# Kernel tuning notes

Measured on AMD Instinct MI355X. Metric: run time of the kernel, lower is better.

## Reference

```python
import jax, jax.numpy as jnp
import numpy as np

SHIFT = 1
EPS = 1e-5

def setup_inputs() -> dict:
    key = jax.random.key(0)
    k1, k2, k3, k4, k5, k6 = jax.random.split(key, 6)
    B, C, H, Wd = 64, 512, 28, 28
    Cout = 512
    return {
        "x": jax.random.normal(k1, (B, C, H, Wd), dtype=jnp.float32),
        "W": jax.random.normal(k2, (Cout, C), dtype=jnp.float32) * 0.05,
        "gamma": jax.random.uniform(k3, (Cout,), dtype=jnp.float32) + 0.5,
        "beta": jax.random.normal(k4, (Cout,), dtype=jnp.float32) * 0.1,
        "running_mean": jax.random.normal(k5, (Cout,), dtype=jnp.float32) * 0.1,
        "running_var": jax.random.uniform(k6, (Cout,), dtype=jnp.float32) + 0.5,
    }

def reference(x, W, gamma, beta, running_mean, running_var):
    # Group-wise spatial shift: split channels into 4 groups, roll each.
    Cg = x.shape[1] // 4
    x1 = jnp.roll(x[:, 0*Cg:1*Cg], -SHIFT, axis=2)  # up
    x2 = jnp.roll(x[:, 1*Cg:2*Cg],  SHIFT, axis=2)  # down
    x3 = jnp.roll(x[:, 2*Cg:3*Cg], -SHIFT, axis=3)  # left
    x4 = jnp.roll(x[:, 3*Cg:4*Cg],  SHIFT, axis=3)  # right
    shifted = jnp.concatenate([x1, x2, x3, x4], axis=1)  # [B,C,H,W]
    # 1x1 conv (no bias) == channel matmul
    y = jnp.einsum('bchw,oc->bohw', shifted, W)
    # BatchNorm (inference: running stats) folded to scale/shift, then ReLU
    scale = gamma * jax.lax.rsqrt(running_var + EPS)
    shift = beta - running_mean * scale
    y = y * scale[None, :, None, None] + shift[None, :, None, None]
    return jnp.maximum(y, 0.0)
```

## Files before the change

kernel.cpp:

```cpp
#include <hip/hip_runtime.h>
#include <hip/hip_bf16.h>

#define BN   64
#define CIN  512
#define COUT 512
#define HW   784
#define NT   128
#define MT   112
#define BK   64
#define TROW 68

typedef __attribute__((ext_vector_type(8))) short short8;
typedef __attribute__((ext_vector_type(4))) float f32x4;

__device__ __forceinline__ unsigned short f2bf(float f) {
    union { float f; unsigned int u; } v; v.f = f;
    unsigned int r = v.u + 0x7fffu + ((v.u >> 16) & 1u);
    return (unsigned short)(r >> 16);
}

__device__ __forceinline__ uint2 pack4(float a, float b, float c, float d) {
    uint2 r;
    r.x = (unsigned int)f2bf(a) | ((unsigned int)f2bf(b) << 16);
    r.y = (unsigned int)f2bf(c) | ((unsigned int)f2bf(d) << 16);
    return r;
}

__device__ __forceinline__ void gl_lds16(const unsigned short* g, unsigned short* l) {
    __builtin_amdgcn_global_load_lds(
        (const __attribute__((address_space(1))) unsigned int*)g,
        (__attribute__((address_space(3))) unsigned int*)l,
        16, 0, 0);
}

__global__ __launch_bounds__(448)
void p1_shift_cvt(const float* __restrict__ x, const float* __restrict__ W,
                  unsigned short* __restrict__ Wb, unsigned short* __restrict__ Xt)
{
    __shared__ unsigned short sT[MT * TROW];
    const int t = threadIdx.x;
    if (blockIdx.z == BN) {
        int wlin = blockIdx.x * 7 + blockIdx.y;
        for (int gi = wlin * 448 + t; gi < (COUT * CIN) / 8; gi += 56 * 448) {
            const float* p = W + (size_t)gi * 8;
            float4 a = *(const float4*)p;
            float4 c = *(const float4*)(p + 4);
            uint2 lo = pack4(a.x, a.y, a.z, a.w);
            uint2 hi = pack4(c.x, c.y, c.z, c.w);
            uint4 v; v.x = lo.x; v.y = lo.y; v.z = hi.x; v.w = hi.y;
            *(uint4*)(Wb + (size_t)gi * 8) = v;
        }
        return;
    }
    const int kk = blockIdx.x;
    const int mt = blockIdx.y;
    const int b  = blockIdx.z;
    const int g  = kk >> 1;
    const int c0 = kk * BK;
    const int hw_base = mt * MT;
    const float* xb = x + (size_t)b * CIN * HW;

    {
        const int cq = t / 28;
        const int mq = t - cq * 28;
        const int hw = hw_base + mq * 4;
        const float* src = xb + (size_t)(c0 + cq * 4) * HW;
        float4 v0, v1, v2, v3;
        if (g < 2) {
            int shw = hw + (g == 0 ? 28 : HW - 28);
            if (shw >= HW) shw -= HW;
            v0 = *(const float4*)(src + 0 * HW + shw);
            v1 = *(const float4*)(src + 1 * HW + shw);
            v2 = *(const float4*)(src + 2 * HW + shw);
            v3 = *(const float4*)(src + 3 * HW + shw);
        } else {
            int h  = hw / 28;
            int w0 = hw - h * 28;
            int base = h * 28;
            #pragma unroll
            for (int j = 0; j < 4; ++j) {
                const float* row = src + j * HW + base;
                float4 a = *(const float4*)(row + w0);
                float4 r;
                if (g == 2) {
                    float ex = row[(w0 + 4 < 28) ? (w0 + 4) : 0];
                    r.x = a.y; r.y = a.z; r.z = a.w; r.w = ex;
                } else {
                    float ex = row[(w0 == 0) ? 27 : (w0 - 1)];
                    r.x = ex; r.y = a.x; r.z = a.y; r.w = a.z;
                }
                if (j == 0) v0 = r; else if (j == 1) v1 = r;
                else if (j == 2) v2 = r; else v3 = r;
            }
        }
        const int m0 = mq * 4;
        const int p  = (cq + mq) % 17;
        *(uint2*)(&sT[(m0 + 0) * TROW + p * 4]) = pack4(v0.x, v1.x, v2.x, v3.x);
        *(uint2*)(&sT[(m0 + 1) * TROW + p * 4]) = pack4(v0.y, v1.y, v2.y, v3.y);
        *(uint2*)(&sT[(m0 + 2) * TROW + p * 4]) = pack4(v0.z, v1.z, v2.z, v3.z);
        *(uint2*)(&sT[(m0 + 3) * TROW + p * 4]) = pack4(v0.w, v1.w, v2.w, v3.w);
    }
    __syncthreads();

    unsigned short* Xb = Xt + ((size_t)(b * 8 + kk) * HW + hw_base) * BK;
    #pragma unroll
    for (int e0 = 0; e0 < 2; ++e0) {
        int ch = t + e0 * 448;
        int m = ch >> 3, j = ch & 7;
        int q4 = m >> 2;
        int p0 = (2 * j + q4) % 17;
        int p1 = (2 * j + 1 + q4) % 17;
        uint2 a = *(const uint2*)(&sT[m * TROW + p0 * 4]);
        uint2 c = *(const uint2*)(&sT[m * TROW + p1 * 4]);
        uint4 v; v.x = a.x; v.y = a.y; v.z = c.x; v.w = c.y;
        *(uint4*)(Xb + (size_t)m * BK + j * 8) = v;
    }
}

__global__ __launch_bounds__(256, 2)
void p2_gemm(const unsigned short* __restrict__ Wb, const unsigned short* __restrict__ Xt,
             const float* __restrict__ gamma, const float* __restrict__ beta,
             const float* __restrict__ rmean, const float* __restrict__ rvar,
             float* __restrict__ out)
{
    __shared__ unsigned short sX[2][MT * BK];

    const int t  = threadIdx.x;
    const int id   = blockIdx.x;
    const int ot   = (id >> 3) & 3;
    const int pair = ((id >> 5) << 3) | (id & 7);
    const int mt   = pair % 7;
    const int b    = pair / 7;
    const int o_base  = ot * NT;
    const int hw_base = mt * MT;
    const int lane = t & 63;
    const int wv   = t >> 6;
    const int m16  = lane & 15;
    const int q    = lane >> 4;

    const unsigned short* Xbase = Xt + ((size_t)(b * 8) * HW + hw_base) * BK;

    auto stage = [&](int kk, int bufi) {
        unsigned short* buf = sX[bufi];
        const unsigned short* Xk = Xbase + (size_t)kk * HW * BK;
        int nci = (wv < 2) ? 4 : 3;
        for (int i = 0; i < nci; ++i) {
            int ci = wv + 4 * i;
            int ch = ci * 64 + lane;
            int hl = ch >> 3, sl = ch & 7;
            int cs = sl ^ (hl & 7);
            gl_lds16(Xk + hl * BK + cs * 8, &buf[ci * 512]);
        }
    };

    const unsigned short* wrow0 = Wb + (size_t)(o_base + wv * 32 + m16) * CIN + q * 8;
    const unsigned short* wrow1 = wrow0 + 16 * CIN;

    f32x4 acc[2][7];
    #pragma unroll
    for (int i = 0; i < 2; ++i)
        #pragma unroll
        for (int j = 0; j < 7; ++j)
            acc[i][j] = (f32x4){0.f, 0.f, 0.f, 0.f};

    short8 wc[2][2], wn[2][2];
    stage(0, 0);
    wc[0][0] = *(const short8*)(wrow0);
    wc[0][1] = *(const short8*)(wrow1);
    wc[1][0] = *(const short8*)(wrow0 + 32);
    wc[1][1] = *(const short8*)(wrow1 + 32);
    __syncthreads();

#define COMPUTE(XS, WF)                                                          \
    {                                                                            \
        const unsigned short* xs = (XS);                                         \
        _Pragma("unroll")                                                        \
        for (int ks = 0; ks < 2; ++ks) {                                         \
            _Pragma("unroll")                                                    \
            for (int bm = 0; bm < 7; ++bm) {                                     \
                int m  = bm * 16 + m16;                                          \
                int lc = ks * 4 + q;                                             \
                int sl = lc ^ (m & 7);                                           \
                short8 bf = *(const short8*)(&xs[m * BK + sl * 8]);              \
                acc[0][bm] = __builtin_amdgcn_mfma_f32_16x16x32_bf16(WF[ks][0], bf, acc[0][bm], 0, 0, 0); \
                acc[1][bm] = __builtin_amdgcn_mfma_f32_16x16x32_bf16(WF[ks][1], bf, acc[1][bm], 0, 0, 0); \
            }                                                                    \
        }                                                                        \
    }

    #pragma unroll 1
    for (int kp = 0; kp < 4; ++kp) {
        {
            const int kn = 2 * kp + 1;
            stage(kn, 1);
            wn[0][0] = *(const short8*)(wrow0 + kn * 64);
            wn[0][1] = *(const short8*)(wrow1 + kn * 64);
            wn[1][0] = *(const short8*)(wrow0 + kn * 64 + 32);
            wn[1][1] = *(const short8*)(wrow1 + kn * 64 + 32);
            COMPUTE(sX[0], wc);
            __syncthreads();
        }
        {
            const int kn = 2 * kp + 2;
            if (kn < 8) {
                stage(kn, 0);
                wc[0][0] = *(const short8*)(wrow0 + kn * 64);
                wc[0][1] = *(const short8*)(wrow1 + kn * 64);
                wc[1][0] = *(const short8*)(wrow0 + kn * 64 + 32);
                wc[1][1] = *(const short8*)(wrow1 + kn * 64 + 32);
            }
            COMPUTE(sX[1], wn);
            __syncthreads();
        }
    }
#undef COMPUTE

    float scl[2][4], shf[2][4];
    #pragma unroll
    for (int bo = 0; bo < 2; ++bo)
        #pragma unroll
        for (int r = 0; r < 4; ++r) {
            int o = o_base + wv * 32 + bo * 16 + q * 4 + r;
            float sc = gamma[o] * rsqrtf(rvar[o] + 1e-5f);
            scl[bo][r] = sc;
            shf[bo][r] = beta[o] - rmean[o] * sc;
        }
    float* outb = out + (size_t)b * COUT * HW;
    #pragma unroll
    for (int bo = 0; bo < 2; ++bo) {
        #pragma unroll
        for (int r = 0; r < 4; ++r) {
            int o = o_base + wv * 32 + bo * 16 + q * 4 + r;
            float* orow = outb + (size_t)o * HW + hw_base + m16;
            #pragma unroll
            for (int bm = 0; bm < 7; ++bm) {
                float y = acc[bo][bm][r] * scl[bo][r] + shf[bo][r];
                y = fmaxf(y, 0.f);
                __builtin_nontemporal_store(y, orow + bm * 16);
            }
        }
    }
}

#define SW_STRIDE 72
#define SX_STRIDE 64
__global__ __launch_bounds__(256, 2)
void shiftconv_fallback(const float* __restrict__ x, const float* __restrict__ Wf,
                        const float* __restrict__ gamma, const float* __restrict__ beta,
                        const float* __restrict__ rmean, const float* __restrict__ rvar,
                        float* __restrict__ out)
{
    __shared__ unsigned short sW[NT * SW_STRIDE];
    __shared__ unsigned short sX[MT * SX_STRIDE];
    const int t = threadIdx.x;
    const int ot = blockIdx.x, mt = blockIdx.y, b = blockIdx.z;
    const int o_base = ot * NT, hw_base = mt * MT;
    const float* xb = x + (size_t)b * CIN * HW;
    const int lane = t & 63, wv = t >> 6, m16 = lane & 15, q = lane >> 4;
    f32x4 acc[2][7];
    #pragma unroll
    for (int i = 0; i < 2; ++i)
        #pragma unroll
        for (int j = 0; j < 7; ++j) acc[i][j] = (f32x4){0.f, 0.f, 0.f, 0.f};
    #pragma unroll
    for (int kk = 0; kk < CIN / BK; ++kk) {
        const int k0 = kk * BK;
        const int g = k0 >> 7;
        #pragma unroll
        for (int e0 = 0; e0 < 2; ++e0) {
            int e = t + e0 * 256;
            if (e < (BK / 4) * (MT / 4)) {
                int cq = e / 28, mq = e - cq * 28;
                int hw = hw_base + mq * 4;
                const float* src = xb + (size_t)(k0 + cq * 4) * HW;
                float4 v0, v1, v2, v3;
                if (g < 2) {
                    int shw = hw + (g == 0 ? 28 : HW - 28);
                    if (shw >= HW) shw -= HW;
                    v0 = *(const float4*)(src + 0 * HW + shw);
                    v1 = *(const float4*)(src + 1 * HW + shw);
                    v2 = *(const float4*)(src + 2 * HW + shw);
                    v3 = *(const float4*)(src + 3 * HW + shw);
                } else {
                    int h = hw / 28, w0 = hw - h * 28, base = h * 28;
                    #pragma unroll
                    for (int j = 0; j < 4; ++j) {
                        const float* row = src + j * HW + base;
                        float4 a = *(const float4*)(row + w0);
                        float4 r;
                        if (g == 2) {
                            float ex = row[(w0 + 4 < 28) ? (w0 + 4) : 0];
                            r.x = a.y; r.y = a.z; r.z = a.w; r.w = ex;
                        } else {
                            float ex = row[(w0 == 0) ? 27 : (w0 - 1)];
                            r.x = ex; r.y = a.x; r.z = a.y; r.w = a.z;
                        }
                        if (j == 0) v0 = r; else if (j == 1) v1 = r;
                        else if (j == 2) v2 = r; else v3 = r;
                    }
                }
                int m0 = mq * 4;
                { int p = (cq + 5 * (m0 + 0)) & 15;
                  *(uint2*)(&sX[(m0 + 0) * SX_STRIDE + p * 4]) = pack4(v0.x, v1.x, v2.x, v3.x); }
                { int p = (cq + 5 * (m0 + 1)) & 15;
                  *(uint2*)(&sX[(m0 + 1) * SX_STRIDE + p * 4]) = pack4(v0.y, v1.y, v2.y, v3.y); }
                { int p = (cq + 5 * (m0 + 2)) & 15;
                  *(uint2*)(&sX[(m0 + 2) * SX_STRIDE + p * 4]) = pack4(v0.z, v1.z, v2.z, v3.z); }
                { int p = (cq + 5 * (m0 + 3)) & 15;
                  *(uint2*)(&sX[(m0 + 3) * SX_STRIDE + p * 4]) = pack4(v0.w, v1.w, v2.w, v3.w); }
            }
        }
        #pragma unroll
        for (int i = 0; i < 4; ++i) {
            int e = t + i * 256;
            int ol = e >> 3, kg = (e & 7) * 8;
            const float* wr = Wf + (size_t)(o_base + ol) * CIN + k0 + kg;
            float4 a = *(const float4*)(wr);
            float4 c = *(const float4*)(wr + 4);
            uint2 lo = pack4(a.x, a.y, a.z, a.w);
            uint2 hi = pack4(c.x, c.y, c.z, c.w);
            uint4 v; v.x = lo.x; v.y = lo.y; v.z = hi.x; v.w = hi.y;
            *(uint4*)(&sW[ol * SW_STRIDE + kg]) = v;
        }
        __syncthreads();
        #pragma unroll
        for (int ks = 0; ks < BK; ks += 32) {
            short8 afrag[2];
            #pragma unroll
            for (int bo = 0; bo < 2; ++bo) {
                int row = wv * 32 + bo * 16 + m16;
                afrag[bo] = *(const short8*)(&sW[row * SW_STRIDE + ks + q * 8]);
            }
            #pragma unroll
            for (int bm = 0; bm < 7; ++bm) {
                int m = bm * 16 + m16;
                int g0 = (ks >> 2) + 2 * q;
                int p0 = (g0 + 5 * m) & 15;
                int p1 = (g0 + 1 + 5 * m) & 15;
                uint2 lo = *(const uint2*)(&sX[m * SX_STRIDE + p0 * 4]);
                uint2 hi = *(const uint2*)(&sX[m * SX_STRIDE + p1 * 4]);
                union { uint2 u2[2]; short8 s; } fb;
                fb.u2[0] = lo; fb.u2[1] = hi;
                acc[0][bm] = __builtin_amdgcn_mfma_f32_16x16x32_bf16(afrag[0], fb.s, acc[0][bm], 0, 0, 0);
                acc[1][bm] = __builtin_amdgcn_mfma_f32_16x16x32_bf16(afrag[1], fb.s, acc[1][bm], 0, 0, 0);
            }
        }
        __syncthreads();
    }
    float scl[2][4], shf[2][4];
    #pragma unroll
    for (int bo = 0; bo < 2; ++bo)
        #pragma unroll
        for (int r = 0; r < 4; ++r) {
            int o = o_base + wv * 32 + bo * 16 + q * 4 + r;
            float sc = gamma[o] * rsqrtf(rvar[o] + 1e-5f);
            scl[bo][r] = sc;
            shf[bo][r] = beta[o] - rmean[o] * sc;
        }
    float* outb = out + (size_t)b * COUT * HW;
    #pragma unroll
    for (int bo = 0; bo < 2; ++bo)
        #pragma unroll
        for (int r = 0; r < 4; ++r) {
            int o = o_base + wv * 32 + bo * 16 + q * 4 + r;
            float* orow = outb + (size_t)o * HW + hw_base + m16;
            #pragma unroll
            for (int bm = 0; bm < 7; ++bm) {
                float y = acc[bo][bm][r] * scl[bo][r] + shf[bo][r];
                y = fmaxf(y, 0.f);
                __builtin_nontemporal_store(y, orow + bm * 16);
            }
        }
}

extern "C" void kernel_launch(void* const* d_in, const int* in_sizes, int n_in,
                              void* d_out, int out_size, void* d_ws, size_t ws_size,
                              hipStream_t stream)
{
    const float* x     = (const float*)d_in[0];
    const float* W     = (const float*)d_in[1];
    const float* gamma = (const float*)d_in[2];
    const float* beta  = (const float*)d_in[3];
    const float* rmean = (const float*)d_in[4];
    const float* rvar  = (const float*)d_in[5];
    float* out = (float*)d_out;

    const size_t wb_bytes = (size_t)COUT * CIN * 2;
    const size_t xt_bytes = (size_t)BN * CIN * HW * 2;
    if (ws_size >= wb_bytes + xt_bytes) {
        unsigned short* Wb = (unsigned short*)d_ws;
        unsigned short* Xt = (unsigned short*)((char*)d_ws + wb_bytes);
        dim3 g1(8, 7, BN + 1);
        p1_shift_cvt<<<g1, 448, 0, stream>>>(x, W, Wb, Xt);
        p2_gemm<<<1792, 256, 0, stream>>>(Wb, Xt, gamma, beta, rmean, rvar, out);
    } else {
        dim3 grid(COUT / NT, HW / MT, BN);
        shiftconv_fallback<<<grid, 256, 0, stream>>>(x, W, gamma, beta, rmean, rvar, out);
    }
}
```

Before: 227.9 us.

## Fuse shift and bf16 conversion into GEMM, covering all output channels per block

New measurement: 237.2 us. 1.04x slower.

```diff
diff --git a/kernel.cpp b/kernel.cpp
--- a/kernel.cpp
+++ b/kernel.cpp
@@ -1,5 +1,4 @@
 #include <hip/hip_runtime.h>
-#include <hip/hip_bf16.h>
 
 #define BN   64
 #define CIN  512
@@ -8,7 +7,7 @@
 #define NT   128
 #define MT   112
 #define BK   64
-#define TROW 68
+#define NKB  (CIN / BK)
 
 typedef __attribute__((ext_vector_type(8))) short short8;
 typedef __attribute__((ext_vector_type(4))) float f32x4;
@@ -26,99 +25,21 @@
     return r;
 }
 
-__device__ __forceinline__ void gl_lds16(const unsigned short* g, unsigned short* l) {
-    __builtin_amdgcn_global_load_lds(
-        (const __attribute__((address_space(1))) unsigned int*)g,
-        (__attribute__((address_space(3))) unsigned int*)l,
-        16, 0, 0);
-}
-
-__global__ __launch_bounds__(448)
-void p1_shift_cvt(const float* __restrict__ x, const float* __restrict__ W,
-                  unsigned short* __restrict__ Wb, unsigned short* __restrict__ Xt)
+__global__ __launch_bounds__(256)
+void p0_wcvt(const float* __restrict__ W, unsigned short* __restrict__ Wb)
 {
-    __shared__ unsigned short sT[MT * TROW];
-    const int t = threadIdx.x;
-    if (blockIdx.z == BN) {
-        int wlin = blockIdx.x * 7 + blockIdx.y;
-        for (int gi = wlin * 448 + t; gi < (COUT * CIN) / 8; gi += 56 * 448) {
-            const float* p = W + (size_t)gi * 8;
-            float4 a = *(const float4*)p;
-            float4 c = *(const float4*)(p + 4);
-            uint2 lo = pack4(a.x, a.y, a.z, a.w);
-            uint2 hi = pack4(c.x, c.y, c.z, c.w);
-            uint4 v; v.x = lo.x; v.y = lo.y; v.z = hi.x; v.w = hi.y;
-            *(uint4*)(Wb + (size_t)gi * 8) = v;
-        }
-        return;
-    }
-    const int kk = blockIdx.x;
-    const int mt = blockIdx.y;
-    const int b  = blockIdx.z;
-    const int g  = kk >> 1;
-    const int c0 = kk * BK;
-    const int hw_base = mt * MT;
-    const float* xb = x + (size_t)b * CIN * HW;
-
-    {
-        const int cq = t / 28;
-        const int mq = t - cq * 28;
-        const int hw = hw_base + mq * 4;
-        const float* src = xb + (size_t)(c0 + cq * 4) * HW;
-        float4 v0, v1, v2, v3;
-        if (g < 2) {
-            int shw = hw + (g == 0 ? 28 : HW - 28);
-            if (shw >= HW) shw -= HW;
-            v0 = *(const float4*)(src + 0 * HW + shw);
-            v1 = *(const float4*)(src + 1 * HW + shw);
-            v2 = *(const float4*)(src + 2 * HW + shw);
-            v3 = *(const float4*)(src + 3 * HW + shw);
-        } else {
-            int h  = hw / 28;
-            int w0 = hw - h * 28;
-            int base = h * 28;
-            #pragma unroll
-            for (int j = 0; j < 4; ++j) {
-                const float* row = src + j * HW + base;
-                float4 a = *(const float4*)(row + w0);
-                float4 r;
-                if (g == 2) {
-                    float ex = row[(w0 + 4 < 28) ? (w0 + 4) : 0];
-                    r.x = a.y; r.y = a.z; r.z = a.w; r.w = ex;
-                } else {
-                    float ex = row[(w0 == 0) ? 27 : (w0 - 1)];
-                    r.x = ex; r.y = a.x; r.z = a.y; r.w = a.z;
-                }
-                if (j == 0) v0 = r; else if (j == 1) v1 = r;
-                else if (j == 2) v2 = r; else v3 = r;
-            }
-        }
-        const int m0 = mq * 4;
-        const int p  = (cq + mq) % 17;
-        *(uint2*)(&sT[(m0 + 0) * TROW + p * 4]) = pack4(v0.x, v1.x, v2.x, v3.x);
-        *(uint2*)(&sT[(m0 + 1) * TROW + p * 4]) = pack4(v0.y, v1.y, v2.y, v3.y);
-        *(uint2*)(&sT[(m0 + 2) * TROW + p * 4]) = pack4(v0.z, v1.z, v2.z, v3.z);
-        *(uint2*)(&sT[(m0 + 3) * TROW + p * 4]) = pack4(v0.w, v1.w, v2.w, v3.w);
-    }
-    __syncthreads();
-
-    unsigned short* Xb = Xt + ((size_t)(b * 8 + kk) * HW + hw_base) * BK;
-    #pragma unroll
-    for (int e0 = 0; e0 < 2; ++e0) {
-        int ch = t + e0 * 448;
-        int m = ch >> 3, j = ch & 7;
-        int q4 = m >> 2;
-        int p0 = (2 * j + q4) % 17;
-        int p1 = (2 * j + 1 + q4) % 17;
-        uint2 a = *(const uint2*)(&sT[m * TROW + p0 * 4]);
-        uint2 c = *(const uint2*)(&sT[m * TROW + p1 * 4]);
-        uint4 v; v.x = a.x; v.y = a.y; v.z = c.x; v.w = c.y;
-        *(uint4*)(Xb + (size_t)m * BK + j * 8) = v;
-    }
-}
-
-__global__ __launch_bounds__(256, 2)
-void p2_gemm(const unsigned short* __restrict__ Wb, const unsigned short* __restrict__ Xt,
+    int gi = blockIdx.x * 256 + threadIdx.x;
+    const float* p = W + (size_t)gi * 8;
+    float4 a = *(const float4*)p;
+    float4 c = *(const float4*)(p + 4);
+    uint2 lo = pack4(a.x, a.y, a.z, a.w);
+    uint2 hi = pack4(c.x, c.y, c.z, c.w);
+    uint4 v; v.x = lo.x; v.y = lo.y; v.z = hi.x; v.w = hi.y;
+    *(uint4*)(Wb + (size_t)gi * 8) = v;
+}
+
+__global__ __launch_bounds__(512, 2)
+void p_fused(const float* __restrict__ x, const unsigned short* __restrict__ Wb,
              const float* __restrict__ gamma, const float* __restrict__ beta,
              const float* __restrict__ rmean, const float* __restrict__ rvar,
              float* __restrict__ out)
@@ -126,50 +47,100 @@
     __shared__ unsigned short sX[2][MT * BK];
 
     const int t  = threadIdx.x;
-    const int id   = blockIdx.x;
-    const int ot   = (id >> 3) & 3;
-    const int pair = ((id >> 5) << 3) | (id & 7);
-    const int mt   = pair % 7;
-    const int b    = pair / 7;
-    const int o_base  = ot * NT;
+    const int id = blockIdx.x;
+    const int mt = id % 7;
+    const int b  = id / 7;
     const int hw_base = mt * MT;
-    const int lane = t & 63;
-    const int wv   = t >> 6;
-    const int m16  = lane & 15;
-    const int q    = lane >> 4;
-
-    const unsigned short* Xbase = Xt + ((size_t)(b * 8) * HW + hw_base) * BK;
-
-    auto stage = [&](int kk, int bufi) {
-        unsigned short* buf = sX[bufi];
-        const unsigned short* Xk = Xbase + (size_t)kk * HW * BK;
-        int nci = (wv < 2) ? 4 : 3;
-        for (int i = 0; i < nci; ++i) {
-            int ci = wv + 4 * i;
-            int ch = ci * 64 + lane;
-            int hl = ch >> 3, sl = ch & 7;
-            int cs = sl ^ (hl & 7);
-            gl_lds16(Xk + hl * BK + cs * 8, &buf[ci * 512]);
+    const int lane = t & 63, wv = t >> 6, m16 = lane & 15, q = lane >> 4;
+    const float* xb = x + (size_t)b * CIN * HW;
+
+    const int cq = t & 15;
+    const int mq = t >> 4;
+    const bool act = (mq < 28);
+    const int hw = hw_base + mq * 4;
+    const int h  = hw / 28;
+    const int w0 = hw - h * 28;
+
+    float4 va0, va1, va2, va3;
+    float  ex0, ex1, ex2, ex3;
+
+    auto loadx = [&](int kk) {
+        if (!act) return;
+        const int g = kk >> 1;
+        const float* src = xb + (size_t)(kk * BK + cq * 4) * HW;
+        if (g < 2) {
+            int shw = hw + (g == 0 ? 28 : HW - 28);
+            if (shw >= HW) shw -= HW;
+            va0 = *(const float4*)(src + 0 * HW + shw);
+            va1 = *(const float4*)(src + 1 * HW + shw);
+            va2 = *(const float4*)(src + 2 * HW + shw);
+            va3 = *(const float4*)(src + 3 * HW + shw);
+        } else {
+            const int base = h * 28;
+            const int wx = (g == 2) ? ((w0 + 4 < 28) ? (w0 + 4) : 0)
+                                    : ((w0 == 0) ? 27 : (w0 - 1));
+            const float* r0 = src + 0 * HW + base;
+            const float* r1 = src + 1 * HW + base;
+            const float* r2 = src + 2 * HW + base;
+            const float* r3 = src + 3 * HW + base;
+            va0 = *(const float4*)(r0 + w0);  ex0 = r0[wx];
+            va1 = *(const float4*)(r1 + w0);  ex1 = r1[wx];
+            va2 = *(const float4*)(r2 + w0);  ex2 = r2[wx];
+            va3 = *(const float4*)(r3 + w0);  ex3 = r3[wx];
         }
     };
 
-    const unsigned short* wrow0 = Wb + (size_t)(o_base + wv * 32 + m16) * CIN + q * 8;
-    const unsigned short* wrow1 = wrow0 + 16 * CIN;
-
-    f32x4 acc[2][7];
-    #pragma unroll
-    for (int i = 0; i < 2; ++i)
+    auto packst = [&](int kk, unsigned short* buf) {
+        if (!act) return;
+        const int g = kk >> 1;
+        float4 r0 = va0, r1 = va1, r2 = va2, r3 = va3;
+        if (g == 2) {
+            r0 = make_float4(va0.y, va0.z, va0.w, ex0);
+            r1 = make_float4(va1.y, va1.z, va1.w, ex1);
+            r2 = make_float4(va2.y, va2.z, va2.w, ex2);
+            r3 = make_float4(va3.y, va3.z, va3.w, ex3);
+        } else if (g == 3) {
+            r0 = make_float4(ex0, va0.x, va0.y, va0.z);
+            r1 = make_float4(ex1, va1.x, va1.y, va1.z);
+            r2 = make_float4(ex2, va2.x, va2.y, va2.z);
+            r3 = make_float4(ex3, va3.x, va3.y, va3.z);
+        }
+        uint2 u0 = pack4(r0.x, r1.x, r2.x, r3.x);
+        uint2 u1 = pack4(r0.y, r1.y, r2.y, r3.y);
+        uint2 u2 = pack4(r0.z, r1.z, r2.z, r3.z);
+        uint2 u3 = pack4(r0.w, r1.w, r2.w, r3.w);
+        const int m0 = mq * 4;
+        const int gr = cq >> 1, hf4 = (cq & 1) * 4;
+        *(uint2*)(&buf[(m0 + 0) * BK + ((gr ^ ((m0 + 0) & 7)) * 8) + hf4]) = u0;
+        *(uint2*)(&buf[(m0 + 1) * BK + ((gr ^ ((m0 + 1) & 7)) * 8) + hf4]) = u1;
+        *(uint2*)(&buf[(m0 + 2) * BK + ((gr ^ ((m0 + 2) & 7)) * 8) + hf4]) = u2;
+        *(uint2*)(&buf[(m0 + 3) * BK + ((gr ^ ((m0 + 3) & 7)) * 8) + hf4]) = u3;
+    };
+
+    const unsigned short* wr0 = Wb + (size_t)(wv * 64 + m16) * CIN + q * 8;
+    const unsigned short* wr1 = wr0 + 16 * CIN;
+    const unsigned short* wr2 = wr0 + 32 * CIN;
+    const unsigned short* wr3 = wr0 + 48 * CIN;
+
+    short8 wc[2][4], wn[2][4];
+#define LOADW(DST, KK)                                  \
+    {   const int ko = (KK) * 64;                       \
+        DST[0][0] = *(const short8*)(wr0 + ko);         \
+        DST[0][1] = *(const short8*)(wr1 + ko);         \
+        DST[0][2] = *(const short8*)(wr2 + ko);         \
+        DST[0][3] = *(const short8*)(wr3 + ko);         \
+        DST[1][0] = *(const short8*)(wr0 + ko + 32);    \
+        DST[1][1] = *(const short8*)(wr1 + ko + 32);    \
+        DST[1][2] = *(const short8*)(wr2 + ko + 32);    \
+        DST[1][3] = *(const short8*)(wr3 + ko + 32);    \
+    }
+
+    f32x4 acc[4][7];
+    #pragma unroll
+    for (int i = 0; i < 4; ++i)
         #pragma unroll
         for (int j = 0; j < 7; ++j)
             acc[i][j] = (f32x4){0.f, 0.f, 0.f, 0.f};
-
-    short8 wc[2][2], wn[2][2];
-    stage(0, 0);
-    wc[0][0] = *(const short8*)(wrow0);
-    wc[0][1] = *(const short8*)(wrow1);
-    wc[1][0] = *(const short8*)(wrow0 + 32);
-    wc[1][1] = *(const short8*)(wrow1 + 32);
-    __syncthreads();
 
 #define COMPUTE(XS, WF)                                                          \
     {                                                                            \
@@ -179,58 +150,63 @@
             _Pragma("unroll")                                                    \
             for (int bm = 0; bm < 7; ++bm) {                                     \
                 int m  = bm * 16 + m16;                                          \
-                int lc = ks * 4 + q;                                             \
-                int sl = lc ^ (m & 7);                                           \
+                int sl = (ks * 4 + q) ^ (m & 7);                                 \
                 short8 bf = *(const short8*)(&xs[m * BK + sl * 8]);              \
                 acc[0][bm] = __builtin_amdgcn_mfma_f32_16x16x32_bf16(WF[ks][0], bf, acc[0][bm], 0, 0, 0); \
                 acc[1][bm] = __builtin_amdgcn_mfma_f32_16x16x32_bf16(WF[ks][1], bf, acc[1][bm], 0, 0, 0); \
+                acc[2][bm] = __builtin_amdgcn_mfma_f32_16x16x32_bf16(WF[ks][2], bf, acc[2][bm], 0, 0, 0); \
+                acc[3][bm] = __builtin_amdgcn_mfma_f32_16x16x32_bf16(WF[ks][3], bf, acc[3][bm], 0, 0, 0); \
             }                                                                    \
         }                                                                        \
     }
+
+    loadx(0);
+    LOADW(wc, 0);
+    packst(0, sX[0]);
+    __syncthreads();
 
     #pragma unroll 1
     for (int kp = 0; kp < 4; ++kp) {
         {
             const int kn = 2 * kp + 1;
-            stage(kn, 1);
-            wn[0][0] = *(const short8*)(wrow0 + kn * 64);
-            wn[0][1] = *(const short8*)(wrow1 + kn * 64);
-            wn[1][0] = *(const short8*)(wrow0 + kn * 64 + 32);
-            wn[1][1] = *(const short8*)(wrow1 + kn * 64 + 32);
+            loadx(kn);
+            LOADW(wn, kn);
             COMPUTE(sX[0], wc);
+            packst(kn, sX[1]);
             __syncthreads();
         }
         {
             const int kn = 2 * kp + 2;
-            if (kn < 8) {
-                stage(kn, 0);
-                wc[0][0] = *(const short8*)(wrow0 + kn * 64);
-                wc[0][1] = *(const short8*)(wrow1 + kn * 64);
-                wc[1][0] = *(const short8*)(wrow0 + kn * 64 + 32);
-                wc[1][1] = *(const short8*)(wrow1 + kn * 64 + 32);
+            if (kn < NKB) {
+                loadx(kn);
+                LOADW(wc, kn);
             }
             COMPUTE(sX[1], wn);
+            if (kn < NKB) {
+                packst(kn, sX[0]);
+            }
             __syncthreads();
         }
     }
 #undef COMPUTE
-
-    float scl[2][4], shf[2][4];
-    #pragma unroll
-    for (int bo = 0; bo < 2; ++bo)
+#undef LOADW
+
+    float scl[4][4], shf[4][4];
+    #pragma unroll
+    for (int bo = 0; bo < 4; ++bo)
         #pragma unroll
         for (int r = 0; r < 4; ++r) {
-            int o = o_base + wv * 32 + bo * 16 + q * 4 + r;
+            int o = wv * 64 + bo * 16 + q * 4 + r;
             float sc = gamma[o] * rsqrtf(rvar[o] + 1e-5f);
             scl[bo][r] = sc;
             shf[bo][r] = beta[o] - rmean[o] * sc;
         }
     float* outb = out + (size_t)b * COUT * HW;
     #pragma unroll
-    for (int bo = 0; bo < 2; ++bo) {
+    for (int bo = 0; bo < 4; ++bo) {
         #pragma unroll
         for (int r = 0; r < 4; ++r) {
-            int o = o_base + wv * 32 + bo * 16 + q * 4 + r;
+            int o = wv * 64 + bo * 16 + q * 4 + r;
             float* orow = outb + (size_t)o * HW + hw_base + m16;
             #pragma unroll
             for (int bm = 0; bm < 7; ++bm) {
@@ -386,13 +362,10 @@
     float* out = (float*)d_out;
 
     const size_t wb_bytes = (size_t)COUT * CIN * 2;
-    const size_t xt_bytes = (size_t)BN * CIN * HW * 2;
-    if (ws_size >= wb_bytes + xt_bytes) {
+    if (ws_size >= wb_bytes) {
         unsigned short* Wb = (unsigned short*)d_ws;
-        unsigned short* Xt = (unsigned short*)((char*)d_ws + wb_bytes);
-        dim3 g1(8, 7, BN + 1);
-        p1_shift_cvt<<<g1, 448, 0, stream>>>(x, W, Wb, Xt);
-        p2_gemm<<<1792, 256, 0, stream>>>(Wb, Xt, gamma, beta, rmean, rvar, out);
+        p0_wcvt<<<dim3(128), dim3(256), 0, stream>>>(W, Wb);
+        p_fused<<<dim3(448), dim3(512), 0, stream>>>(x, Wb, gamma, beta, rmean, rvar, out);
     } else {
         dim3 grid(COUT / NT, HW / MT, BN);
         shiftconv_fallback<<<grid, 256, 0, stream>>>(x, W, gamma, beta, rmean, rvar, out);
```

## Pre-swizzle operands into MFMA fragment layout and load directly to registers

Applied to the files above, without the earlier changes.

Result: slower. 258.7 us (+13.5%).

```diff
diff --git a/kernel.cpp b/kernel.cpp
--- a/kernel.cpp
+++ b/kernel.cpp
@@ -1,5 +1,4 @@
 #include <hip/hip_runtime.h>
-#include <hip/hip_bf16.h>
 
 #define BN   64
 #define CIN  512
@@ -8,6 +7,7 @@
 #define NT   128
 #define MT   112
 #define BK   64
+#define NKB  (CIN / BK)
 #define TROW 68
 
 typedef __attribute__((ext_vector_type(8))) short short8;
@@ -26,32 +26,25 @@
     return r;
 }
 
-__device__ __forceinline__ void gl_lds16(const unsigned short* g, unsigned short* l) {
-    __builtin_amdgcn_global_load_lds(
-        (const __attribute__((address_space(1))) unsigned int*)g,
-        (__attribute__((address_space(3))) unsigned int*)l,
-        16, 0, 0);
+__global__ __launch_bounds__(256)
+void p0_wcvt(const float* __restrict__ W, unsigned short* __restrict__ Wb)
+{
+    int gi = blockIdx.x * 256 + threadIdx.x;
+    const float* p = W + (size_t)gi * 8;
+    float4 a = *(const float4*)p;
+    float4 c = *(const float4*)(p + 4);
+    uint2 lo = pack4(a.x, a.y, a.z, a.w);
+    uint2 hi = pack4(c.x, c.y, c.z, c.w);
+    uint4 v; v.x = lo.x; v.y = lo.y; v.z = hi.x; v.w = hi.y;
+    int o = gi >> 6, j = gi & 63;
+    *(uint4*)(Wb + (size_t)(o >> 4) * 8192 + j * 128 + (o & 15) * 8) = v;
 }
 
 __global__ __launch_bounds__(448)
-void p1_shift_cvt(const float* __restrict__ x, const float* __restrict__ W,
-                  unsigned short* __restrict__ Wb, unsigned short* __restrict__ Xt)
+void p1_shift_cvt(const float* __restrict__ x, unsigned short* __restrict__ Xt)
 {
     __shared__ unsigned short sT[MT * TROW];
     const int t = threadIdx.x;
-    if (blockIdx.z == BN) {
-        int wlin = blockIdx.x * 7 + blockIdx.y;
-        for (int gi = wlin * 448 + t; gi < (COUT * CIN) / 8; gi += 56 * 448) {
-            const float* p = W + (size_t)gi * 8;
-            float4 a = *(const float4*)p;
-            float4 c = *(const float4*)(p + 4);
-            uint2 lo = pack4(a.x, a.y, a.z, a.w);
-            uint2 hi = pack4(c.x, c.y, c.z, c.w);
-            uint4 v; v.x = lo.x; v.y = lo.y; v.z = hi.x; v.w = hi.y;
-            *(uint4*)(Wb + (size_t)gi * 8) = v;
-        }
-        return;
-    }
     const int kk = blockIdx.x;
     const int mt = blockIdx.y;
     const int b  = blockIdx.z;
@@ -102,18 +95,18 @@
     }
     __syncthreads();
 
-    unsigned short* Xb = Xt + ((size_t)(b * 8 + kk) * HW + hw_base) * BK;
+    unsigned short* Xb = Xt + (size_t)((b * NKB + kk) * 7 + mt) * 7168;
     #pragma unroll
     for (int e0 = 0; e0 < 2; ++e0) {
         int ch = t + e0 * 448;
         int m = ch >> 3, j = ch & 7;
         int q4 = m >> 2;
-        int p0 = (2 * j + q4) % 17;
-        int p1 = (2 * j + 1 + q4) % 17;
-        uint2 a = *(const uint2*)(&sT[m * TROW + p0 * 4]);
-        uint2 c = *(const uint2*)(&sT[m * TROW + p1 * 4]);
+        int pa = (2 * j + q4) % 17;
+        int pb = (2 * j + 1 + q4) % 17;
+        uint2 a = *(const uint2*)(&sT[m * TROW + pa * 4]);
+        uint2 c = *(const uint2*)(&sT[m * TROW + pb * 4]);
         uint4 v; v.x = a.x; v.y = a.y; v.z = c.x; v.w = c.y;
-        *(uint4*)(Xb + (size_t)m * BK + j * 8) = v;
+        *(uint4*)(Xb + (m >> 4) * 1024 + (j >> 2) * 512 + (m & 15) * 32 + (j & 3) * 8) = v;
     }
 }
 
@@ -123,114 +116,71 @@
              const float* __restrict__ rmean, const float* __restrict__ rvar,
              float* __restrict__ out)
 {
-    __shared__ unsigned short sX[2][MT * BK];
-
     const int t  = threadIdx.x;
     const int id   = blockIdx.x;
-    const int ot   = (id >> 3) & 3;
-    const int pair = ((id >> 5) << 3) | (id & 7);
+    const int ot   = (id >> 3) & 1;
+    const int pair = ((id >> 4) << 3) | (id & 7);
     const int mt   = pair % 7;
     const int b    = pair / 7;
-    const int o_base  = ot * NT;
+    const int o_base  = ot * 256;
     const int hw_base = mt * MT;
-    const int lane = t & 63;
-    const int wv   = t >> 6;
-    const int m16  = lane & 15;
-    const int q    = lane >> 4;
-
-    const unsigned short* Xbase = Xt + ((size_t)(b * 8) * HW + hw_base) * BK;
-
-    auto stage = [&](int kk, int bufi) {
-        unsigned short* buf = sX[bufi];
-        const unsigned short* Xk = Xbase + (size_t)kk * HW * BK;
-        int nci = (wv < 2) ? 4 : 3;
-        for (int i = 0; i < nci; ++i) {
-            int ci = wv + 4 * i;
-            int ch = ci * 64 + lane;
-            int hl = ch >> 3, sl = ch & 7;
-            int cs = sl ^ (hl & 7);
-            gl_lds16(Xk + hl * BK + cs * 8, &buf[ci * 512]);
-        }
-    };
-
-    const unsigned short* wrow0 = Wb + (size_t)(o_base + wv * 32 + m16) * CIN + q * 8;
-    const unsigned short* wrow1 = wrow0 + 16 * CIN;
-
-    f32x4 acc[2][7];
-    #pragma unroll
-    for (int i = 0; i < 2; ++i)
+    const int lane = t & 63, wv = t >> 6, m16 = lane & 15, q = lane >> 4;
+
+    const unsigned short* Xs = Xt + (size_t)((b * NKB) * 7 + mt) * 7168 + m16 * 32 + q * 8;
+    const unsigned short* Wf = Wb + (size_t)((o_base + wv * 64) >> 4) * 8192 + q * 128 + m16 * 8;
+
+    f32x4 acc[4][7];
+    #pragma unroll
+    for (int i = 0; i < 4; ++i)
         #pragma unroll
         for (int j = 0; j < 7; ++j)
             acc[i][j] = (f32x4){0.f, 0.f, 0.f, 0.f};
 
-    short8 wc[2][2], wn[2][2];
-    stage(0, 0);
-    wc[0][0] = *(const short8*)(wrow0);
-    wc[0][1] = *(const short8*)(wrow1);
-    wc[1][0] = *(const short8*)(wrow0 + 32);
-    wc[1][1] = *(const short8*)(wrow1 + 32);
-    __syncthreads();
-
-#define COMPUTE(XS, WF)                                                          \
-    {                                                                            \
-        const unsigned short* xs = (XS);                                         \
-        _Pragma("unroll")                                                        \
-        for (int ks = 0; ks < 2; ++ks) {                                         \
-            _Pragma("unroll")                                                    \
-            for (int bm = 0; bm < 7; ++bm) {                                     \
-                int m  = bm * 16 + m16;                                          \
-                int lc = ks * 4 + q;                                             \
-                int sl = lc ^ (m & 7);                                           \
-                short8 bf = *(const short8*)(&xs[m * BK + sl * 8]);              \
-                acc[0][bm] = __builtin_amdgcn_mfma_f32_16x16x32_bf16(WF[ks][0], bf, acc[0][bm], 0, 0, 0); \
-                acc[1][bm] = __builtin_amdgcn_mfma_f32_16x16x32_bf16(WF[ks][1], bf, acc[1][bm], 0, 0, 0); \
-            }                                                                    \
-        }                                                                        \
-    }
-
-    #pragma unroll 1
-    for (int kp = 0; kp < 4; ++kp) {
-        {
-            const int kn = 2 * kp + 1;
-            stage(kn, 1);
-            wn[0][0] = *(const short8*)(wrow0 + kn * 64);
-            wn[0][1] = *(const short8*)(wrow1 + kn * 64);
-            wn[1][0] = *(const short8*)(wrow0 + kn * 64 + 32);
-            wn[1][1] = *(const short8*)(wrow1 + kn * 64 + 32);
-            COMPUTE(sX[0], wc);
-            __syncthreads();
-        }
-        {
-            const int kn = 2 * kp + 2;
-            if (kn < 8) {
-                stage(kn, 0);
-                wc[0][0] = *(const short8*)(wrow0 + kn * 64);
-                wc[0][1] = *(const short8*)(wrow1 + kn * 64);
-                wc[1][0] = *(const short8*)(wrow0 + kn * 64 + 32);
-                wc[1][1] = *(const short8*)(wrow1 + kn * 64 + 32);
-            }
-            COMPUTE(sX[1], wn);
-            __syncthreads();
-        }
-    }
-#undef COMPUTE
-
-    float scl[2][4], shf[2][4];
-    #pragma unroll
-    for (int bo = 0; bo < 2; ++bo)
+#define MFMA16(A, B, C) __builtin_amdgcn_mfma_f32_16x16x32_bf16((A), (B), (C), 0, 0, 0)
+    #pragma unroll
+    for (int kk = 0; kk < NKB; ++kk) {
+        const unsigned short* xk = Xs + (size_t)kk * (7 * 7168);
+        const unsigned short* wk = Wf + kk * 1024;
+        short8 w00 = *(const short8*)(wk + 0 * 8192);
+        short8 w01 = *(const short8*)(wk + 1 * 8192);
+        short8 w02 = *(const short8*)(wk + 2 * 8192);
+        short8 w03 = *(const short8*)(wk + 3 * 8192);
+        short8 w10 = *(const short8*)(wk + 0 * 8192 + 512);
+        short8 w11 = *(const short8*)(wk + 1 * 8192 + 512);
+        short8 w12 = *(const short8*)(wk + 2 * 8192 + 512);
+        short8 w13 = *(const short8*)(wk + 3 * 8192 + 512);
+        #pragma unroll
+        for (int bm = 0; bm < 7; ++bm) {
+            short8 b0 = *(const short8*)(xk + bm * 1024);
+            short8 b1 = *(const short8*)(xk + bm * 1024 + 512);
+            acc[0][bm] = MFMA16(w00, b0, acc[0][bm]);
+            acc[1][bm] = MFMA16(w01, b0, acc[1][bm]);
+            acc[2][bm] = MFMA16(w02, b0, acc[2][bm]);
+            acc[3][bm] = MFMA16(w03, b0, acc[3][bm]);
+            acc[0][bm] = MFMA16(w10, b1, acc[0][bm]);
+            acc[1][bm] = MFMA16(w11, b1, acc[1][bm]);
+            acc[2][bm] = MFMA16(w12, b1, acc[2][bm]);
+            acc[3][bm] = MFMA16(w13, b1, acc[3][bm]);
+        }
+    }
+#undef MFMA16
+
+    float scl[4][4], shf[4][4];
+    #pragma unroll
+    for (int bo = 0; bo < 4; ++bo)
         #pragma unroll
         for (int r = 0; r < 4; ++r) {
-            int o = o_base + wv * 32 + bo * 16 + q * 4 + r;
+            int o = o_base + wv * 64 + bo * 16 + q * 4 + r;
             float sc = gamma[o] * rsqrtf(rvar[o] + 1e-5f);
             scl[bo][r] = sc;
             shf[bo][r] = beta[o] - rmean[o] * sc;
         }
     float* outb = out + (size_t)b * COUT * HW;
     #pragma unroll
-    for (int bo = 0; bo < 2; ++bo) {
+    for (int bo = 0; bo < 4; ++bo) {
         #pragma unroll
         for (int r = 0; r < 4; ++r) {
-            int o = o_base + wv * 32 + bo * 16 + q * 4 + r;
+            int o = o_base + wv * 64 + bo * 16 + q * 4 + r;
             float* orow = outb + (size_t)o * HW + hw_base + m16;
             #pragma unroll
             for (int bm = 0; bm < 7; ++bm) {
@@ -390,9 +340,9 @@
     if (ws_size >= wb_bytes + xt_bytes) {
         unsigned short* Wb = (unsigned short*)d_ws;
         unsigned short* Xt = (unsigned short*)((char*)d_ws + wb_bytes);
-        dim3 g1(8, 7, BN + 1);
-        p1_shift_cvt<<<g1, 448, 0, stream>>>(x, W, Wb, Xt);
-        p2_gemm<<<1792, 256, 0, stream>>>(Wb, Xt, gamma, beta, rmean, rvar, out);
+        p0_wcvt<<<dim3(128), dim3(256), 0, stream>>>(W, Wb);
+        p1_shift_cvt<<<dim3(8, 7, BN), dim3(448), 0, stream>>>(x, Xt);
+        p2_gemm<<<dim3(896), dim3(256), 0, stream>>>(Wb, Xt, gamma, beta, rmean, rvar, out);
     } else {
         dim3 grid(COUT / NT, HW / MT, BN);
         shiftconv_fallback<<<grid, 256, 0, stream>>>(x, W, gamma, beta, rmean, rvar, out);
```
